# Performance work log

Hardware: AMD Instinct MI355X
Metric: run time of the kernel (lower is better)

Reference implementation:

```python
import jax, jax.numpy as jnp
import numpy as np

# SMPL-X kinematic tree (55 joints): 22 body, jaw, 2 eyes, 15 left-hand, 15 right-hand
PARENTS = np.array([-1, 0, 0, 0, 1, 2, 3, 4, 5, 6, 7, 8, 9, 9, 9, 12, 13, 14, 16, 17, 18, 19,
                    15, 15, 15,
                    20, 25, 26, 20, 28, 29, 20, 31, 32, 20, 34, 35, 20, 37, 38,
                    21, 40, 41, 21, 43, 44, 21, 46, 47, 21, 49, 50, 21, 52, 53])
V = 10475   # SMPL-X vertex count
J = 55      # joints
NB = 10     # betas
PF = 54 * 9 # pose-feature dim
B, L = 4, 128


def axis_angle_to_matrix(aa):
    # aa: (..., 3) -> (..., 3, 3) via Rodrigues' formula
    angle = jnp.sqrt(jnp.sum(aa * aa, axis=-1, keepdims=True) + 1e-12)  # (...,1)
    axis = aa / angle
    x, y, z = axis[..., 0], axis[..., 1], axis[..., 2]
    zero = jnp.zeros_like(x)
    K = jnp.stack([jnp.stack([zero, -z, y], -1),
                   jnp.stack([z, zero, -x], -1),
                   jnp.stack([-y, x, zero], -1)], axis=-2)           # (...,3,3)
    s = jnp.sin(angle)[..., None]
    c = jnp.cos(angle)[..., None]
    eye = jnp.eye(3, dtype=aa.dtype)
    outer = axis[..., :, None] * axis[..., None, :]
    return c * eye + s * K + (1.0 - c) * outer


def batch_rigid_transform(rot_mats, joints):
    # rot_mats: (..., J, 3, 3), joints: (..., J, 3) -> rel_transforms (..., J, 4, 4)
    rel = jnp.concatenate([joints[..., :1, :],
                           joints[..., 1:, :] - joints[..., PARENTS[1:], :]], axis=-2)
    top = jnp.concatenate([rot_mats, rel[..., None]], axis=-1)        # (...,J,3,4)
    bottom = jnp.broadcast_to(jnp.array([0., 0., 0., 1.], top.dtype),
                              top.shape[:-2] + (1, 4))
    tmats = jnp.concatenate([top, bottom], axis=-2)                   # (...,J,4,4)
    chain = [tmats[..., 0, :, :]]
    for i in range(1, J):  # fixed 55-joint tree dependency
        chain.append(chain[PARENTS[i]] @ tmats[..., i, :, :])
    T = jnp.stack(chain, axis=-3)                                     # (...,J,4,4)
    corr = jnp.einsum('...jcd,...jd->...jc', T[..., :3, :3], joints)
    return T.at[..., :3, 3].add(-corr)


def setup_inputs() -> dict:
    key = jax.random.key(0)
    ks = jax.random.split(key, 11)
    w = jax.random.uniform(ks[8], (V, J), dtype=jnp.float32)
    lbs_weights = w / jnp.sum(w, axis=-1, keepdims=True)
    return {
        'body_pose': 0.3 * jax.random.normal(ks[0], (B, L, 63), jnp.float32),
        'betas': jax.random.normal(ks[1], (B, L, NB), jnp.float32),
        'global_orient': 0.3 * jax.random.normal(ks[2], (B, L, 3), jnp.float32),
        'transl': jax.random.normal(ks[3], (B, L, 3), jnp.float32),
        'v_template': 0.5 * jax.random.normal(ks[4], (V, 3), jnp.float32),
        'shapedirs': 0.01 * jax.random.normal(ks[5], (V, 3, NB), jnp.float32),
        'posedirs': 0.01 * jax.random.normal(ks[6], (PF, V, 3), jnp.float32),
        'lbs_weights': lbs_weights,
        'J_template': 0.3 * jax.random.normal(ks[7], (J, 3), jnp.float32),
        'J_shapedirs': 0.01 * jax.random.normal(ks[9], (J, 3, NB), jnp.float32),
        'other_default_pose': 0.1 * jax.random.normal(ks[10], (99,), jnp.float32),
    }


def reference(body_pose, betas, global_orient, transl, v_template, shapedirs,
              posedirs, lbs_weights, J_template, J_shapedirs, other_default_pose):
    prefix = body_pose.shape[:-1]
    odp = jnp.broadcast_to(other_default_pose, prefix + (99,))
    full_pose = jnp.concatenate([global_orient, body_pose, odp], axis=-1)  # (B,L,165)
    rot_mats = axis_angle_to_matrix(full_pose.reshape(prefix + (J, 3)))    # (B,L,55,3,3)
    # fast skeleton
    joints = J_template + jnp.einsum('...k,jck->...jc', betas, J_shapedirs)  # (B,L,55,3)
    A = batch_rigid_transform(rot_mats, joints)                              # (B,L,55,4,4)
    eye = jnp.eye(3, dtype=rot_mats.dtype)
    pose_feature = (rot_mats[..., 1:, :, :] - eye).reshape(prefix + (PF,))
    v_posed = (v_template
               + jnp.einsum('...k,vck->...vc', betas, shapedirs)
               + jnp.einsum('...k,kvc->...vc', pose_feature, posedirs))      # (B,L,V,3)
    T = jnp.einsum('vj,...jcd->...vcd', lbs_weights, A)                      # (B,L,V,4,4)
    verts = (jnp.einsum('...vcd,...vd->...vc', T[..., :3, :3], v_posed)
             + T[..., :3, 3])
    return verts + transl[..., None, :]
```

## Files before the change

kernel.cpp:

```cpp
#include <hip/hip_runtime.h>

#define V_CNT   10475
#define N3      31425
#define NPAD    31488
#define J_CNT   55
#define NBETA   10
#define KP      512
#define NFRAMES 512
#define BM      64
#define BNC     192
#define VTILES  164
#define FTILES  8
#define RPK_BLOCKS (492 * 8)

typedef __attribute__((ext_vector_type(8))) __bf16 bf16x8;
typedef __attribute__((ext_vector_type(8))) unsigned short ushort8;
typedef __attribute__((ext_vector_type(4))) float f32x4;

__device__ __forceinline__ unsigned short f2bf(float f) {
    unsigned u = __float_as_uint(f);
    u += 0x7fff + ((u >> 16) & 1);
    return (unsigned short)(u >> 16);
}
__device__ __forceinline__ float bf2f(unsigned short s) {
    return __uint_as_float(((unsigned)s) << 16);
}
__device__ __forceinline__ void gl_lds16(const void* g, void* l) {
    auto gp = (const __attribute__((address_space(1))) unsigned int*)(uintptr_t)g;
    auto lp = (__attribute__((address_space(3))) unsigned int*)(unsigned int)(uintptr_t)l;
    __builtin_amdgcn_global_load_lds(gp, lp, 16, 0, 0);
}

__device__ __constant__ int c_parents[J_CNT] = {
    -1, 0, 0, 0, 1, 2, 3, 4, 5, 6, 7, 8, 9, 9, 9, 12, 13, 14, 16, 17, 18, 19,
    15, 15, 15,
    20, 25, 26, 20, 28, 29, 20, 31, 32, 20, 34, 35, 20, 37, 38,
    21, 40, 41, 21, 43, 44, 21, 46, 47, 21, 49, 50, 21, 52, 53};

__global__ __launch_bounds__(256) void prep_kernel(
    const float* __restrict__ posedirs, const float* __restrict__ shapedirs,
    const float* __restrict__ v_template, unsigned short* __restrict__ B_pack,
    const float* __restrict__ body_pose, const float* __restrict__ betas,
    const float* __restrict__ global_orient, const float* __restrict__ J_template,
    const float* __restrict__ J_shapedirs, const float* __restrict__ odp,
    unsigned short* __restrict__ pf_ext, unsigned short* __restrict__ A_bf)
{
    const int rb = blockIdx.x;
    const int tid = threadIdx.x;

    __shared__ float R_s[J_CNT][9];
    __shared__ float j_s[J_CNT][3];
    __shared__ float G_s[J_CNT][12];

    if (rb < RPK_BLOCKS) {
        const int n0 = (rb % 492) * 64;
        const int k0 = (rb / 492) * 64;
        const int nl = tid >> 2;
        const int kh = tid & 3;
        const int ng = n0 + nl;
        ushort8 v0, v1;
#pragma unroll
        for (int j = 0; j < 16; j++) {
            int kgl = k0 + kh * 16 + j;
            float v = 0.0f;
            if (ng < N3) {
                if (kgl < 486)       v = posedirs[(size_t)kgl * N3 + ng];
                else if (kgl < 496)  v = shapedirs[ng * NBETA + (kgl - 486)];
                else if (kgl == 496) v = v_template[ng];
            }
            if (j < 8) v0[j] = f2bf(v);
            else       v1[j - 8] = f2bf(v);
        }
        unsigned short* dst = &B_pack[(size_t)(n0 + nl) * KP + k0 + kh * 16];
        *(ushort8*)(dst)     = v0;
        *(ushort8*)(dst + 8) = v1;
        return;
    }

    const int n = rb - RPK_BLOCKS;
    const int lane = tid;

    if (lane < J_CNT) {
        float aa0, aa1, aa2;
        if (lane == 0) {
            aa0 = global_orient[n * 3 + 0];
            aa1 = global_orient[n * 3 + 1];
            aa2 = global_orient[n * 3 + 2];
        } else if (lane < 22) {
            int o = n * 63 + (lane - 1) * 3;
            aa0 = body_pose[o]; aa1 = body_pose[o + 1]; aa2 = body_pose[o + 2];
        } else {
            int o = (lane - 22) * 3;
            aa0 = odp[o]; aa1 = odp[o + 1]; aa2 = odp[o + 2];
        }
        float ang = sqrtf(aa0 * aa0 + aa1 * aa1 + aa2 * aa2 + 1e-12f);
        float inv = 1.0f / ang;
        float ax = aa0 * inv, ay = aa1 * inv, az = aa2 * inv;
        float s = sinf(ang), c = cosf(ang), cc = 1.0f - c;
        float R[9];
        R[0] = c + cc * ax * ax;        R[1] = -s * az + cc * ax * ay;  R[2] = s * ay + cc * ax * az;
        R[3] = s * az + cc * ax * ay;   R[4] = c + cc * ay * ay;        R[5] = -s * ax + cc * ay * az;
        R[6] = -s * ay + cc * ax * az;  R[7] = s * ax + cc * ay * az;   R[8] = c + cc * az * az;
#pragma unroll
        for (int k = 0; k < 9; k++) R_s[lane][k] = R[k];
#pragma unroll
        for (int cd = 0; cd < 3; cd++) {
            float acc = J_template[lane * 3 + cd];
#pragma unroll
            for (int k = 0; k < NBETA; k++)
                acc += betas[n * NBETA + k] * J_shapedirs[(lane * 3 + cd) * NBETA + k];
            j_s[lane][cd] = acc;
        }
        if (lane >= 1) {
#pragma unroll
            for (int e = 0; e < 9; e++)
                pf_ext[n * KP + (lane - 1) * 9 + e] =
                    f2bf(R[e] - ((e == 0 || e == 4 || e == 8) ? 1.0f : 0.0f));
        }
    }
    if (lane == 55) {
#pragma unroll
        for (int b = 0; b < NBETA; b++) pf_ext[n * KP + 486 + b] = f2bf(betas[n * NBETA + b]);
        pf_ext[n * KP + 496] = 0x3F80;
    }
    if (lane == 56) {
        for (int k = 497; k < KP; k++) pf_ext[n * KP + k] = 0;
    }
    __syncthreads();
    if (lane == 0) {
        for (int r = 0; r < 3; r++) {
            G_s[0][r * 4 + 0] = R_s[0][r * 3 + 0];
            G_s[0][r * 4 + 1] = R_s[0][r * 3 + 1];
            G_s[0][r * 4 + 2] = R_s[0][r * 3 + 2];
            G_s[0][r * 4 + 3] = j_s[0][r];
        }
        for (int i = 1; i < J_CNT; i++) {
            int p = c_parents[i];
            float rel0 = j_s[i][0] - j_s[p][0];
            float rel1 = j_s[i][1] - j_s[p][1];
            float rel2 = j_s[i][2] - j_s[p][2];
            for (int r = 0; r < 3; r++) {
                float g0 = G_s[p][r * 4 + 0], g1 = G_s[p][r * 4 + 1], g2 = G_s[p][r * 4 + 2];
                G_s[i][r * 4 + 0] = g0 * R_s[i][0] + g1 * R_s[i][3] + g2 * R_s[i][6];
                G_s[i][r * 4 + 1] = g0 * R_s[i][1] + g1 * R_s[i][4] + g2 * R_s[i][7];
                G_s[i][r * 4 + 2] = g0 * R_s[i][2] + g1 * R_s[i][5] + g2 * R_s[i][8];
                G_s[i][r * 4 + 3] = g0 * rel0 + g1 * rel1 + g2 * rel2 + G_s[p][r * 4 + 3];
            }
        }
    }
    __syncthreads();
    if (lane < 64) {
        float vals[12];
#pragma unroll
        for (int r = 0; r < 12; r++) vals[r] = 0.0f;
        if (lane < J_CNT) {
            const float jx = j_s[lane][0], jy = j_s[lane][1], jz = j_s[lane][2];
#pragma unroll
            for (int r = 0; r < 3; r++) {
                float g0 = G_s[lane][r * 4 + 0], g1 = G_s[lane][r * 4 + 1], g2 = G_s[lane][r * 4 + 2];
                vals[r * 4 + 0] = g0;
                vals[r * 4 + 1] = g1;
                vals[r * 4 + 2] = g2;
                vals[r * 4 + 3] = G_s[lane][r * 4 + 3] - (g0 * jx + g1 * jy + g2 * jz);
            }
        }
#pragma unroll
        for (int r = 0; r < 12; r++)
            A_bf[(n * 12 + r) * 64 + lane] = f2bf(vals[r]);
    }
}

__global__ __launch_bounds__(256, 2) void gemm_kernel(
    const unsigned short* __restrict__ pf_ext, const unsigned short* __restrict__ B_pack,
    const unsigned short* __restrict__ A_bf, const float* __restrict__ lbs_weights,
    const float* __restrict__ transl, float* __restrict__ out)
{
    __shared__ __align__(128) unsigned char smem[74496];
    unsigned char* pf_b0 = smem;
    unsigned char* pf_b1 = smem + 8192;
    unsigned char* B_b0  = smem + 16384;
    unsigned char* B_b1  = smem + 40960;
    unsigned char* w_b   = smem + 65536;
    float* tr_s          = (float*)(smem + 73728);
    unsigned short* vp_s = (unsigned short*)(smem + 16384);
    float* rst           = (float*)(smem + 41472);

    const int tid = threadIdx.x;
    const int w = tid >> 6, l = tid & 63;
    const int wm = w >> 1, wn = w & 1;

    const int bid = blockIdx.x;
    const int group = bid >> 6, gi = bid & 63;
    int vt, ft;
    if (group < 20) { vt = group * 8 + (gi & 7); ft = gi >> 3; }
    else            { vt = 160 + (gi & 3);       ft = gi >> 2; }
    const int f0 = ft * BM;
    const int v00 = vt * 64;
    const int n0c = vt * BNC;

    const unsigned char* pfg = (const unsigned char*)pf_ext + (size_t)f0 * (KP * 2);
    const unsigned char* Bg  = (const unsigned char*)B_pack + (size_t)n0c * (KP * 2);

#define STAGE_KS(ks, pfd, Bd)                                                              \
    {                                                                                      \
        const int kb = (ks) * 128;                                                         \
        _Pragma("unroll")                                                                  \
        for (int i = 0; i < 2; i++) {                                                      \
            int row0 = w * 16 + i * 8;                                                     \
            int row = row0 + (l >> 3);                                                     \
            const unsigned char* src = pfg + (size_t)row * (KP * 2) + kb +                 \
                                       (((l & 7) ^ (l >> 3)) * 16);                        \
            gl_lds16(src, (pfd) + row0 * 128);                                             \
        }                                                                                  \
        _Pragma("unroll")                                                                  \
        for (int i = 0; i < 6; i++) {                                                      \
            int row0 = i * 32 + w * 8;                                                     \
            int row = row0 + (l >> 3);                                                     \
            const unsigned char* src = Bg + (size_t)row * (KP * 2) + kb +                  \
                                       (((l & 7) ^ (l >> 3)) * 16);                        \
            gl_lds16(src, (Bd) + row0 * 128);                                              \
        }                                                                                  \
    }

    f32x4 acc[2][6];
#pragma unroll
    for (int m = 0; m < 2; m++)
#pragma unroll
        for (int nn = 0; nn < 6; nn++) acc[m][nn] = (f32x4){0.f, 0.f, 0.f, 0.f};

    STAGE_KS(0, pf_b0, B_b0);
    STAGE_KS(1, pf_b1, B_b1);
    asm volatile("s_waitcnt vmcnt(8)" ::: "memory");
    __builtin_amdgcn_sched_barrier(0);
    __builtin_amdgcn_s_barrier();

#pragma unroll
    for (int ks = 0; ks < 8; ks++) {
        unsigned char* pfc = (ks & 1) ? pf_b1 : pf_b0;
        unsigned char* Bc  = (ks & 1) ? B_b1 : B_b0;
#pragma unroll
        for (int ksub = 0; ksub < 2; ksub++) {
            bf16x8 a[2], b[6];
#pragma unroll
            for (int m = 0; m < 2; m++) {
                int f = wm * 32 + m * 16 + (l & 15);
                int off = f * 128 + ((ksub * 64 + (l >> 4) * 16) ^ ((f & 7) << 4));
                a[m] = *(const bf16x8*)(pfc + off);
            }
#pragma unroll
            for (int nn = 0; nn < 6; nn++) {
                int col = wn * 96 + nn * 16 + (l & 15);
                int off = col * 128 + ((ksub * 64 + (l >> 4) * 16) ^ ((col & 7) << 4));
                b[nn] = *(const bf16x8*)(Bc + off);
            }
#pragma unroll
            for (int m = 0; m < 2; m++)
#pragma unroll
                for (int nn = 0; nn < 6; nn++)
                    acc[m][nn] = __builtin_amdgcn_mfma_f32_16x16x32_bf16(a[m], b[nn], acc[m][nn], 0, 0, 0);
        }
        __builtin_amdgcn_sched_barrier(0);
        __builtin_amdgcn_s_barrier();
        if (ks < 6) {
            STAGE_KS(ks + 2, pfc, Bc);
        }
        if (ks < 7) {
            if (ks < 6) asm volatile("s_waitcnt vmcnt(8)" ::: "memory");
            else        asm volatile("s_waitcnt vmcnt(0)" ::: "memory");
            __builtin_amdgcn_sched_barrier(0);
            __builtin_amdgcn_s_barrier();
        }
    }
#undef STAGE_KS

    {
        int v = tid >> 2, jg = tid & 3;
        int vg = v00 + v;
#pragma unroll
        for (int h = 0; h < 2; h++) {
            ushort8 val;
#pragma unroll
            for (int e = 0; e < 8; e++) {
                int j = jg * 16 + h * 8 + e;
                float f = (vg < V_CNT && j < J_CNT) ? lbs_weights[vg * J_CNT + j] : 0.0f;
                val[e] = f2bf(f);
            }
            int chunk = (jg * 2 + h) ^ (v & 7);
            *(ushort8*)(w_b + v * 128 + chunk * 16) = val;
        }
    }
    if (tid < 192) tr_s[tid] = transl[f0 * 3 + tid];

#pragma unroll
    for (int m = 0; m < 2; m++)
#pragma unroll
        for (int nn = 0; nn < 6; nn++)
#pragma unroll
            for (int e = 0; e < 4; e++) {
                int f = wm * 32 + m * 16 + (l >> 4) * 4 + e;
                int col = wn * 96 + nn * 16 + (l & 15);
                vp_s[f * 196 + col] = f2bf(acc[m][nn][e]);
            }
    __syncthreads();

    const unsigned char* Ab = (const unsigned char*)A_bf;
    float res[3][8][2];
#pragma unroll
    for (int c = 0; c < 3; c++) {
        f32x4 acc2[8][2];
#pragma unroll
        for (int m = 0; m < 8; m++)
#pragma unroll
            for (int nn = 0; nn < 2; nn++) acc2[m][nn] = (f32x4){0.f, 0.f, 0.f, 0.f};
#pragma unroll
        for (int ksub = 0; ksub < 2; ksub++) {
            bf16x8 bw[2];
#pragma unroll
            for (int nn = 0; nn < 2; nn++) {
                int v = wn * 32 + nn * 16 + (l & 15);
                int off = v * 128 + ((ksub * 64 + (l >> 4) * 16) ^ ((v & 7) << 4));
                bw[nn] = *(const bf16x8*)(w_b + off);
            }
#pragma unroll
            for (int m = 0; m < 8; m++) {
                int row16 = l & 15;
                int f_rel = m * 4 + (row16 >> 2);
                int rr = row16 & 3;
                const unsigned char* asrc = Ab +
                    ((size_t)((f0 + wm * 32 + f_rel) * 12 + c * 4 + rr)) * 128 +
                    ksub * 64 + (l >> 4) * 16;
                bf16x8 af = *(const bf16x8*)asrc;
                acc2[m][0] = __builtin_amdgcn_mfma_f32_16x16x32_bf16(af, bw[0], acc2[m][0], 0, 0, 0);
                acc2[m][1] = __builtin_amdgcn_mfma_f32_16x16x32_bf16(af, bw[1], acc2[m][1], 0, 0, 0);
            }
        }
#pragma unroll
        for (int m = 0; m < 8; m++)
#pragma unroll
            for (int nn = 0; nn < 2; nn++) {
                int f_rel = wm * 32 + m * 4 + (l >> 4);
                int vloc = wn * 32 + nn * 16 + (l & 15);
                float d0 = bf2f(vp_s[f_rel * 196 + vloc * 3 + 0]);
                float d1 = bf2f(vp_s[f_rel * 196 + vloc * 3 + 1]);
                float d2 = bf2f(vp_s[f_rel * 196 + vloc * 3 + 2]);
                f32x4 tt = acc2[m][nn];
                res[c][m][nn] = tt[0] * d0 + tt[1] * d1 + tt[2] * d2 + tt[3] + tr_s[f_rel * 3 + c];
            }
    }

    const int olim = N3 - v00 * 3;
#pragma unroll
    for (int chunk = 0; chunk < 2; chunk++) {
        __syncthreads();
        if (wm == chunk) {
#pragma unroll
            for (int m = 0; m < 8; m++)
#pragma unroll
                for (int nn = 0; nn < 2; nn++) {
                    int r = m * 4 + (l >> 4);
                    int colv = (wn * 32 + nn * 16 + (l & 15)) * 3;
#pragma unroll
                    for (int c = 0; c < 3; c++)
                        rst[r * 200 + colv + c] = res[c][m][nn];
                }
        }
        __syncthreads();
        size_t base = ((size_t)(f0 + chunk * 32) * V_CNT + v00) * 3;
#pragma unroll
        for (int k = 0; k < 24; k++) {
            int i = tid + k * 256;
            int r = i / 192;
            int o = i - r * 192;
            if (o < olim)
                out[base + (size_t)r * N3 + o] = rst[r * 200 + o];
        }
    }
}

extern "C" void kernel_launch(void* const* d_in, const int* in_sizes, int n_in,
                              void* d_out, int out_size, void* d_ws, size_t ws_size,
                              hipStream_t stream)
{
    const float* body_pose     = (const float*)d_in[0];
    const float* betas         = (const float*)d_in[1];
    const float* global_orient = (const float*)d_in[2];
    const float* transl        = (const float*)d_in[3];
    const float* v_template    = (const float*)d_in[4];
    const float* shapedirs     = (const float*)d_in[5];
    const float* posedirs      = (const float*)d_in[6];
    const float* lbs_weights   = (const float*)d_in[7];
    const float* J_template    = (const float*)d_in[8];
    const float* J_shapedirs   = (const float*)d_in[9];
    const float* odp           = (const float*)d_in[10];
    float* out = (float*)d_out;

    unsigned short* B_pack = (unsigned short*)d_ws;
    unsigned short* pf_ext = (unsigned short*)((char*)d_ws + 32243712);
    unsigned short* A_bf   = (unsigned short*)((char*)d_ws + 32243712 + 524288);

    prep_kernel<<<RPK_BLOCKS + NFRAMES, 256, 0, stream>>>(
        posedirs, shapedirs, v_template, B_pack,
        body_pose, betas, global_orient, J_template, J_shapedirs, odp,
        pf_ext, A_bf);

    gemm_kernel<<<VTILES * FTILES, 256, 0, stream>>>(pf_ext, B_pack, A_bf, lbs_weights,
                                                     transl, out);
}
```

Before: 117.3 us.

## Split fused pose-blend GEMM and skinning into two kernels via global buffer

Splits the fused kernel into two. The first computes the pose-blend GEMM and writes bf16 posed vertices to a global workspace buffer. The second reloads them and applies the LBS-weight skinning and translation. This cuts the shared-memory footprint of each kernel and may improve occupancy or scheduling. In exchange it adds a global round trip of roughly 32MB (write plus read) and one extra kernel launch.

```diff
diff --git a/kernel.cpp b/kernel.cpp
--- a/kernel.cpp
+++ b/kernel.cpp
@@ -170,20 +170,16 @@
     }
 }
 
-__global__ __launch_bounds__(256, 2) void gemm_kernel(
+__global__ __launch_bounds__(256, 2) void gemm1_kernel(
     const unsigned short* __restrict__ pf_ext, const unsigned short* __restrict__ B_pack,
-    const unsigned short* __restrict__ A_bf, const float* __restrict__ lbs_weights,
-    const float* __restrict__ transl, float* __restrict__ out)
+    unsigned short* __restrict__ vp_g)
 {
-    __shared__ __align__(128) unsigned char smem[74496];
+    __shared__ __align__(128) unsigned char smem[65536];
     unsigned char* pf_b0 = smem;
     unsigned char* pf_b1 = smem + 8192;
     unsigned char* B_b0  = smem + 16384;
     unsigned char* B_b1  = smem + 40960;
-    unsigned char* w_b   = smem + 65536;
-    float* tr_s          = (float*)(smem + 73728);
     unsigned short* vp_s = (unsigned short*)(smem + 16384);
-    float* rst           = (float*)(smem + 41472);
 
     const int tid = threadIdx.x;
     const int w = tid >> 6, l = tid & 63;
@@ -195,7 +191,6 @@
     if (group < 20) { vt = group * 8 + (gi & 7); ft = gi >> 3; }
     else            { vt = 160 + (gi & 3);       ft = gi >> 2; }
     const int f0 = ft * BM;
-    const int v00 = vt * 64;
     const int n0c = vt * BNC;
 
     const unsigned char* pfg = (const unsigned char*)pf_ext + (size_t)f0 * (KP * 2);
@@ -273,6 +268,55 @@
     }
 #undef STAGE_KS
 
+#pragma unroll
+    for (int m = 0; m < 2; m++)
+#pragma unroll
+        for (int nn = 0; nn < 6; nn++)
+#pragma unroll
+            for (int e = 0; e < 4; e++) {
+                int f = wm * 32 + m * 16 + (l >> 4) * 4 + e;
+                int col = wn * 96 + nn * 16 + (l & 15);
+                vp_s[f * 196 + col] = f2bf(acc[m][nn][e]);
+            }
+    __syncthreads();
+#pragma unroll
+    for (int k = 0; k < 6; k++) {
+        int i = tid + k * 256;
+        int r = i / 24;
+        int c8 = i - r * 24;
+        ushort8 val;
+#pragma unroll
+        for (int j = 0; j < 8; j++) val[j] = vp_s[r * 196 + c8 * 8 + j];
+        *(ushort8*)(&vp_g[(size_t)(f0 + r) * NPAD + n0c + c8 * 8]) = val;
+    }
+}
+
+__global__ __launch_bounds__(256) void gemm2_kernel(
+    const unsigned short* __restrict__ vp_g, const unsigned short* __restrict__ A_bf,
+    const float* __restrict__ lbs_weights, const float* __restrict__ transl,
+    float* __restrict__ out)
+{
+    __shared__ __align__(128) unsigned char smem[34560];
+    unsigned short* vp_s = (unsigned short*)(smem);
+    unsigned char* w_b   = smem + 25600;
+    float* tr_s          = (float*)(smem + 33792);
+    float* rst           = (float*)(smem);
+
+    const int tid = threadIdx.x;
+    const int w = tid >> 6, l = tid & 63;
+    const int wm = w >> 1, wn = w & 1;
+    const int f0 = blockIdx.y * BM;
+    const int v00 = blockIdx.x * 64;
+    const int n0c = blockIdx.x * BNC;
+
+#pragma unroll
+    for (int k = 0; k < 6; k++) {
+        int i = tid + k * 256;
+        int r = i / 24;
+        int c8 = i - r * 24;
+        ushort8 val = *(const ushort8*)(&vp_g[(size_t)(f0 + r) * NPAD + n0c + c8 * 8]);
+        *(ushort8*)(&vp_s[r * 196 + c8 * 8]) = val;
+    }
     {
         int v = tid >> 2, jg = tid & 3;
         int vg = v00 + v;
@@ -290,17 +334,6 @@
         }
     }
     if (tid < 192) tr_s[tid] = transl[f0 * 3 + tid];
-
-#pragma unroll
-    for (int m = 0; m < 2; m++)
-#pragma unroll
-        for (int nn = 0; nn < 6; nn++)
-#pragma unroll
-            for (int e = 0; e < 4; e++) {
-                int f = wm * 32 + m * 16 + (l >> 4) * 4 + e;
-                int col = wn * 96 + nn * 16 + (l & 15);
-                vp_s[f * 196 + col] = f2bf(acc[m][nn][e]);
-            }
     __syncthreads();
 
     const unsigned char* Ab = (const unsigned char*)A_bf;
@@ -397,12 +430,15 @@
     unsigned short* B_pack = (unsigned short*)d_ws;
     unsigned short* pf_ext = (unsigned short*)((char*)d_ws + 32243712);
     unsigned short* A_bf   = (unsigned short*)((char*)d_ws + 32243712 + 524288);
+    unsigned short* vp_g   = (unsigned short*)((char*)d_ws + 33554432);
 
     prep_kernel<<<RPK_BLOCKS + NFRAMES, 256, 0, stream>>>(
         posedirs, shapedirs, v_template, B_pack,
         body_pose, betas, global_orient, J_template, J_shapedirs, odp,
         pf_ext, A_bf);
 
-    gemm_kernel<<<VTILES * FTILES, 256, 0, stream>>>(pf_ext, B_pack, A_bf, lbs_weights,
-                                                     transl, out);
-}
+    gemm1_kernel<<<VTILES * FTILES, 256, 0, stream>>>(pf_ext, B_pack, vp_g);
+
+    dim3 g2(VTILES, FTILES);
+    gemm2_kernel<<<g2, 256, 0, stream>>>(vp_g, A_bf, lbs_weights, transl, out);
+}
```

New measurement: 151.6 us. +29.3%, slower.
